# Performance work log

Hardware: AMD Instinct MI355X
Metric: run time of the kernel (lower is better)

Reference implementation:

```python
import jax, jax.numpy as jnp
import numpy as np

DPITCH_RANGE = 24.0
SCALE = 1.0


def setup_inputs() -> dict:
    key = jax.random.key(0)
    ks = jax.random.split(key, 10)
    B, T, ND, SD, H = 512, 1024, 64, 3, 256
    inp_size = ND + SD  # 67
    w = lambda k, shape: (jax.random.normal(k, shape, jnp.float32) * 0.05)
    return {
        "noise": jax.random.normal(ks[0], (B, T, ND), jnp.float32),
        "gap_duration": jax.random.uniform(ks[1], (B, T + 1, SD - 1), dtype=jnp.float32),
        "W_ih": w(ks[2], (4 * H, inp_size)),
        "W_hh": w(ks[3], (4 * H, H)),
        "b_ih": w(ks[4], (4 * H,)),
        "b_hh": w(ks[5], (4 * H,)),
        "W1": w(ks[6], (H, H)),
        "b1": w(ks[7], (H,)),
        "W2": w(ks[8], (1, H)),
        "b2": w(ks[9], (1,)),
    }


def reference(noise, gap_duration, W_ih, W_hh, b_ih, b_hh, W1, b1, W2, b2):
    B, T, _ = noise.shape
    H = W_hh.shape[1]

    def head(out):  # Linear -> Tanh -> Linear -> Tanh, scaled to deltapitch
        hdn = jnp.tanh(out @ W1.T + b1)
        return jnp.tanh(hdn @ W2.T + b2) * (DPITCH_RANGE * SCALE)

    def lstm_cell(h, c, x):  # torch LSTM gate order: i, f, g, o
        gates = x @ W_ih.T + b_ih + h @ W_hh.T + b_hh
        i, f, g, o = jnp.split(gates, 4, axis=-1)
        c = jax.nn.sigmoid(f) * c + jax.nn.sigmoid(i) * jnp.tanh(g)
        h = jax.nn.sigmoid(o) * jnp.tanh(c)
        return h, c

    def step(carry, inp):
        out, h, c = carry
        n_t, gap_t = inp  # [B, ND], [B, SD-1]
        x = jnp.concatenate([gap_t, head(out)], axis=-1)  # [B, SD]
        h, c = lstm_cell(h, c, jnp.concatenate([x, n_t], axis=-1))
        return (h, h, c), x

    z = jnp.zeros((B, H), noise.dtype)
    (out, _, _), xs = jax.lax.scan(
        step, (z, z, z),
        (noise.transpose(1, 0, 2), gap_duration[:, :T].transpose(1, 0, 2)))
    x_last = jnp.concatenate([gap_duration[:, T], head(out)], axis=-1)
    return jnp.concatenate([xs.transpose(1, 0, 2), x_last[:, None, :]], axis=1)
```

## Files before the change

### kernel.cpp

```cpp
#include <hip/hip_runtime.h>
#include <stdint.h>
#include <stddef.h>

typedef __bf16 bf16x8 __attribute__((ext_vector_type(8)));
typedef float f32x4 __attribute__((ext_vector_type(4)));

#define MFMA16(a, b, c) __builtin_amdgcn_mfma_f32_16x16x32_bf16((a), (b), (c), 0, 0, 0)

#define TSTEPS 1024
#define NDIM   64
#define NKC    10
#define NGT    64
#define MB     16
#define GROUPS 32
#define SLICES 8

#define GOFF    ((size_t)0)
#define GBYTES  ((size_t)NGT * NKC * 1024)
#define W1OFF   (GOFF + GBYTES)
#define W1BYTES ((size_t)16 * 8 * 1024)
#define BOFF    (W1OFF + W1BYTES)
#define XOFF    (BOFF + 4096)
#define XBYTES  ((size_t)256 * 2 * 512 * 4)
#define WSNEED  (XOFF + XBYTES)

__device__ __forceinline__ uint16_t f2bf(float f) {
    union { float f; uint32_t u; } v; v.f = f;
    return (uint16_t)((v.u + 0x7FFFu + ((v.u >> 16) & 1u)) >> 16);
}
__device__ __forceinline__ float fsig(float x) { return 1.0f / (1.0f + __expf(-x)); }
__device__ __forceinline__ float ftanh(float x) { return 2.0f / (1.0f + __expf(-2.0f * x)) - 1.0f; }

__device__ __forceinline__ void bar_lgkm() {
    asm volatile("s_waitcnt lgkmcnt(0)" ::: "memory");
    __builtin_amdgcn_s_barrier();
    asm volatile("" ::: "memory");
}

__global__ void prep_gates(const float* __restrict__ W_ih, const float* __restrict__ W_hh,
                           char* __restrict__ ws) {
    int F = blockIdx.x;
    int T = F / NKC, kc = F - T * NKC;
    int l = threadIdx.x;
    int row  = 16 * T + (l & 15);
    int unit = row >> 2, gt = row & 3;
    int orig = gt * 256 + unit;
    uint32_t w[4];
#pragma unroll
    for (int p = 0; p < 4; ++p) {
        float v[2];
#pragma unroll
        for (int e = 0; e < 2; ++e) {
            int k = 32 * kc + 8 * (l >> 4) + 2 * p + e;
            v[e] = (k < 64) ? W_ih[orig * 67 + 3 + k] : W_hh[orig * 256 + (k - 64)];
        }
        w[p] = (uint32_t)f2bf(v[0]) | ((uint32_t)f2bf(v[1]) << 16);
    }
    *(uint4*)(ws + GOFF + (size_t)F * 1024 + (size_t)l * 16) = make_uint4(w[0], w[1], w[2], w[3]);
}

__global__ void prep_w1(const float* __restrict__ W1, char* __restrict__ ws) {
    int F = blockIdx.x;
    int T = F / 8, kc = F - T * 8;
    int l = threadIdx.x;
    int row = 16 * T + (l & 15);
    uint32_t w[4];
#pragma unroll
    for (int p = 0; p < 4; ++p) {
        int k = 32 * kc + 8 * (l >> 4) + 2 * p;
        w[p] = (uint32_t)f2bf(W1[row * 256 + k]) | ((uint32_t)f2bf(W1[row * 256 + k + 1]) << 16);
    }
    *(uint4*)(ws + W1OFF + (size_t)F * 1024 + (size_t)l * 16) = make_uint4(w[0], w[1], w[2], w[3]);
}

__global__ void prep_small(const float* __restrict__ b_ih, const float* __restrict__ b_hh,
                           char* __restrict__ ws) {
    int t = threadIdx.x;
    float* sb = (float*)(ws + BOFF);
    if (t < 1024) {
        int unit = t >> 2, gt = t & 3;
        int orig = gt * 256 + unit;
        sb[t] = b_ih[orig] + b_hh[orig];
    }
}

__global__ __launch_bounds__(512, 2) void lstm_main(
        const float* __restrict__ noise, const float* __restrict__ gap,
        const float* __restrict__ W_ih, const float* __restrict__ b1p,
        const float* __restrict__ W2p, const float* __restrict__ b2p,
        char* __restrict__ ws, float* __restrict__ out) {
    __shared__ uint16_t act[MB * 320];
    __shared__ float dp_part[16][9];
    __shared__ float gxy[16][2];

    const int tid  = threadIdx.x;
    const int w    = tid >> 6;
    const int lane = tid & 63;
    const int q    = lane >> 4;
    const int col  = lane & 15;
    const int g    = blockIdx.x >> 3;
    const int s    = blockIdx.x & 7;
    const int b0   = g * MB;
    const int swz  = (col & 7) << 3;

    const uint4* gfr  = (const uint4*)(ws + GOFF);
    const uint4* w1fr = (const uint4*)(ws + W1OFF);
    const float* bias = (const float*)(ws + BOFF);
    uint32_t* pay = (uint32_t*)(ws + XOFF);

    for (int i = tid; i < MB * 320; i += 512) act[i] = 0;

    const int T = 8 * s + w;
    uint4 gw[NKC];
#pragma unroll
    for (int kc = 0; kc < NKC; ++kc) gw[kc] = gfr[(size_t)(T * NKC + kc) * 64 + lane];
    uint4 w1w[16];
#pragma unroll
    for (int i = 0; i < 2; ++i)
#pragma unroll
        for (int kc = 0; kc < 8; ++kc)
            w1w[i * 8 + kc] = w1fr[(size_t)((2 * w + i) * 8 + kc) * 64 + lane];

    const int rb = 16 * T + 4 * q;
    const float bI = bias[rb], bF = bias[rb + 1], bG = bias[rb + 2], bO = bias[rb + 3];
    float wx0[4], wx1[4], wx2[4];
#pragma unroll
    for (int r = 0; r < 4; ++r) {
        int row = rb + r;
        int orig = (row & 3) * 256 + (row >> 2);
        wx0[r] = W_ih[orig * 67 + 0];
        wx1[r] = W_ih[orig * 67 + 1];
        wx2[r] = W_ih[orig * 67 + 2] * 24.0f;
    }
    float b1r[8], w2r[8];
#pragma unroll
    for (int a = 0; a < 2; ++a)
#pragma unroll
        for (int r = 0; r < 4; ++r) {
            int row = 32 * w + 16 * a + 4 * q + r;
            b1r[4 * a + r] = b1p[row];
            w2r[4 * a + r] = W2p[row];
        }
    const float b2v = b2p[0];

    const int nbr = tid >> 5, nj = (tid & 31) * 2;
    const float* nptr = noise + (size_t)(b0 + nbr) * TSTEPS * NDIM + nj;
    float2 npf = *(const float2*)nptr;
    const bool xlead = (w == 7 && lane < 16);
    float2 gpf = make_float2(0.f, 0.f);
    if (xlead) gpf = *(const float2*)(gap + (size_t)(b0 + col) * (TSTEPS + 1) * 2);

    float creg = 0.f;
    const f32x4 fz = {0.f, 0.f, 0.f, 0.f};
    const int myidx = g * 8 + s;
    const int myunit = 32 * s + 4 * w + q;

    __syncthreads();

#pragma unroll 1
    for (int t = 0; t <= TSTEPS; ++t) {
        if (t < TSTEPS) {
            uint32_t nv = (uint32_t)f2bf(npf.x) | ((uint32_t)f2bf(npf.y) << 16);
            int sw = (nbr & 7) << 3;
            *(uint32_t*)&act[nbr * 320 + (nj ^ sw)] = nv;
            if (t + 1 < TSTEPS) npf = *(const float2*)(nptr + (size_t)(t + 1) * NDIM);
        }
        if (xlead) {
            gxy[col][0] = gpf.x; gxy[col][1] = gpf.y;
            if (s == 0) {
                float* o = out + ((size_t)(b0 + col) * (TSTEPS + 1) + t) * 3;
                o[0] = gpf.x; o[1] = gpf.y;
            }
            if (t < TSTEPS)
                gpf = *(const float2*)(gap + ((size_t)(b0 + col) * (TSTEPS + 1) + (t + 1)) * 2);
        }
        if (t > 0) {
            const unsigned tag = (unsigned)t;
            const int par = t & 1;
            unsigned pend = 0x7f;
            uint32_t vv[7];
            do {
#pragma unroll
                for (int pi = 0; pi < 7; ++pi)
                    if (pend & (1u << pi)) {
                        int p = (s + 1 + pi) & 7;
                        vv[pi] = __hip_atomic_load(
                            &pay[(((g * 8 + p) * 2 + par) << 9) + 64 * w + lane],
                            __ATOMIC_RELAXED, __HIP_MEMORY_SCOPE_AGENT);
                    }
#pragma unroll
                for (int pi = 0; pi < 7; ++pi)
                    if ((pend & (1u << pi)) && (vv[pi] >> 16) == tag) {
                        int p = (s + 1 + pi) & 7;
                        int u = 32 * p + 4 * w + q;
                        act[col * 320 + ((64 + u) ^ swz)] = (uint16_t)vv[pi];
                        pend &= ~(1u << pi);
                    }
            } while (pend);
        }
        bar_lgkm();

        f32x4 h0 = fz, h1 = fz;
#pragma unroll
        for (int kc = 0; kc < 8; ++kc) {
            bf16x8 bv = *(const bf16x8*)&act[col * 320 + ((64 + 32 * kc + 8 * q) ^ swz)];
            h0 = MFMA16(__builtin_bit_cast(bf16x8, w1w[kc]),     bv, h0);
            h1 = MFMA16(__builtin_bit_cast(bf16x8, w1w[8 + kc]), bv, h1);
        }
        float part = 0.f;
#pragma unroll
        for (int r = 0; r < 4; ++r) {
            part += ftanh(h0[r] + b1r[r])     * w2r[r];
            part += ftanh(h1[r] + b1r[4 + r]) * w2r[4 + r];
        }
        part += __shfl_xor(part, 16);
        part += __shfl_xor(part, 32);
        if (q == 0) dp_part[col][w] = part;
        bar_lgkm();

        const float* dpp = &dp_part[col][0];
        float inner = b2v + ((dpp[0] + dpp[1]) + (dpp[2] + dpp[3]))
                          + ((dpp[4] + dpp[5]) + (dpp[6] + dpp[7]));
        float tdp = ftanh(inner);

        if (t == TSTEPS) {
            if (s == 0 && w == 0 && q == 0)
                out[((size_t)(b0 + col) * (TSTEPS + 1) + t) * 3 + 2] = 24.0f * tdp;
            break;
        }

        f32x4 ga = fz;
#pragma unroll
        for (int kc = 0; kc < NKC; ++kc) {
            bf16x8 bv = *(const bf16x8*)&act[col * 320 + ((32 * kc + 8 * q) ^ swz)];
            ga = MFMA16(__builtin_bit_cast(bf16x8, gw[kc]), bv, ga);
        }
        const float g0 = gxy[col][0], g1 = gxy[col][1];
        float ii = ga[0] + bI + wx0[0] * g0 + wx1[0] * g1 + wx2[0] * tdp;
        float ff = ga[1] + bF + wx0[1] * g0 + wx1[1] * g1 + wx2[1] * tdp;
        float gg = ga[2] + bG + wx0[2] * g0 + wx1[2] * g1 + wx2[2] * tdp;
        float oo = ga[3] + bO + wx0[3] * g0 + wx1[3] * g1 + wx2[3] * tdp;
        float cn = fsig(ff) * creg + fsig(ii) * ftanh(gg);
        creg = cn;
        float hv = fsig(oo) * ftanh(cn);
        uint16_t hb = f2bf(hv);
        __hip_atomic_store(&pay[((myidx * 2 + ((t + 1) & 1)) << 9) + 64 * w + lane],
                           ((uint32_t)(t + 1) << 16) | (uint32_t)hb,
                           __ATOMIC_RELAXED, __HIP_MEMORY_SCOPE_AGENT);
        act[col * 320 + ((64 + myunit) ^ swz)] = hb;
        if (s == 0 && w == 0 && q == 0)
            out[((size_t)(b0 + col) * (TSTEPS + 1) + t) * 3 + 2] = 24.0f * tdp;
        bar_lgkm();
    }
}

extern "C" void kernel_launch(void* const* d_in, const int* in_sizes, int n_in,
                              void* d_out, int out_size, void* d_ws, size_t ws_size,
                              hipStream_t stream) {
    (void)in_sizes; (void)n_in; (void)out_size;
    if (ws_size < WSNEED) return;

    const float* noise = (const float*)d_in[0];
    const float* gap   = (const float*)d_in[1];
    const float* W_ih  = (const float*)d_in[2];
    const float* W_hh  = (const float*)d_in[3];
    const float* b_ih  = (const float*)d_in[4];
    const float* b_hh  = (const float*)d_in[5];
    const float* W1    = (const float*)d_in[6];
    const float* b1    = (const float*)d_in[7];
    const float* W2    = (const float*)d_in[8];
    const float* b2    = (const float*)d_in[9];
    char*  ws  = (char*)d_ws;
    float* out = (float*)d_out;

    hipMemsetAsync(ws + XOFF, 0, XBYTES, stream);
    hipLaunchKernelGGL(prep_gates, dim3(NGT * NKC), dim3(64), 0, stream, W_ih, W_hh, ws);
    hipLaunchKernelGGL(prep_w1,    dim3(16 * 8),    dim3(64), 0, stream, W1, ws);
    hipLaunchKernelGGL(prep_small, dim3(1), dim3(1024), 0, stream, b_ih, b_hh, ws);
    hipLaunchKernelGGL(lstm_main,  dim3(GROUPS * SLICES), dim3(512), 0, stream,
                       noise, gap, W_ih, b1, W2, b2, ws, out);
}
```

Before: 3.132 ms.

## Halve slices per batch group and double-buffer state to drop a barrier per step

Each batch group of 16 rows is now split across 4 workgroups instead of 8. Each wave computes two gate tiles, which cuts the number of peers each workgroup must poll per timestep from 7 to 3, and peer payloads are read as 64-bit atomic loads. The shared activation, noise, gap and partial buffers are double-buffered by timestep parity, so the barrier at the end of each step is removed and the head and gate MFMAs run in one interleaved loop. In exchange each workgroup does twice the gate MFMA work per step and holds more registers, and only 128 workgroups are launched.

After: 6.981 ms. 2.23x slower.

```diff
diff --git a/kernel.cpp b/kernel.cpp
--- a/kernel.cpp
+++ b/kernel.cpp
@@ -13,7 +13,7 @@
 #define NGT    64
 #define MB     16
 #define GROUPS 32
-#define SLICES 8
+#define SLICES 4
 
 #define GOFF    ((size_t)0)
 #define GBYTES  ((size_t)NGT * NKC * 1024)
@@ -21,8 +21,8 @@
 #define W1BYTES ((size_t)16 * 8 * 1024)
 #define BOFF    (W1OFF + W1BYTES)
 #define XOFF    (BOFF + 4096)
-#define XBYTES  ((size_t)256 * 2 * 512 * 4)
-#define WSNEED  (XOFF + XBYTES)
+#define PAYB    ((size_t)GROUPS * SLICES * 2 * 1024 * 4)
+#define WSNEED  (XOFF + PAYB)
 
 __device__ __forceinline__ uint16_t f2bf(float f) {
     union { float f; uint32_t u; } v; v.f = f;
@@ -89,17 +89,19 @@
         const float* __restrict__ W_ih, const float* __restrict__ b1p,
         const float* __restrict__ W2p, const float* __restrict__ b2p,
         char* __restrict__ ws, float* __restrict__ out) {
-    __shared__ uint16_t act[MB * 320];
-    __shared__ float dp_part[16][9];
-    __shared__ float gxy[16][2];
+    __shared__ uint16_t hfrag[2][16 * 256];
+    __shared__ uint16_t actn[2][16 * 64];
+    __shared__ float dp_part[2][16][9];
+    __shared__ float gxy[2][16][2];
 
     const int tid  = threadIdx.x;
     const int w    = tid >> 6;
     const int lane = tid & 63;
     const int q    = lane >> 4;
     const int col  = lane & 15;
-    const int g    = blockIdx.x >> 3;
-    const int s    = blockIdx.x & 7;
+    const int n    = blockIdx.x;
+    const int g    = n >> 2;
+    const int s    = n & 3;
     const int b0   = g * MB;
     const int swz  = (col & 7) << 3;
 
@@ -108,12 +110,15 @@
     const float* bias = (const float*)(ws + BOFF);
     uint32_t* pay = (uint32_t*)(ws + XOFF);
 
-    for (int i = tid; i < MB * 320; i += 512) act[i] = 0;
-
-    const int T = 8 * s + w;
-    uint4 gw[NKC];
-#pragma unroll
-    for (int kc = 0; kc < NKC; ++kc) gw[kc] = gfr[(size_t)(T * NKC + kc) * 64 + lane];
+    for (int i = tid; i < 16 * 256; i += 512) hfrag[0][i] = 0;
+
+    const int T0 = 16 * s + 2 * w;
+    uint4 gw0[NKC], gw1[NKC];
+#pragma unroll
+    for (int kc = 0; kc < NKC; ++kc) {
+        gw0[kc] = gfr[(size_t)(T0 * NKC + kc) * 64 + lane];
+        gw1[kc] = gfr[(size_t)((T0 + 1) * NKC + kc) * 64 + lane];
+    }
     uint4 w1w[16];
 #pragma unroll
     for (int i = 0; i < 2; ++i)
@@ -121,16 +126,19 @@
         for (int kc = 0; kc < 8; ++kc)
             w1w[i * 8 + kc] = w1fr[(size_t)((2 * w + i) * 8 + kc) * 64 + lane];
 
-    const int rb = 16 * T + 4 * q;
-    const float bI = bias[rb], bF = bias[rb + 1], bG = bias[rb + 2], bO = bias[rb + 3];
-    float wx0[4], wx1[4], wx2[4];
-#pragma unroll
-    for (int r = 0; r < 4; ++r) {
-        int row = rb + r;
-        int orig = (row & 3) * 256 + (row >> 2);
-        wx0[r] = W_ih[orig * 67 + 0];
-        wx1[r] = W_ih[orig * 67 + 1];
-        wx2[r] = W_ih[orig * 67 + 2] * 24.0f;
+    float bb[2][4], wxa[2][4], wxb[2][4], wxc[2][4];
+#pragma unroll
+    for (int i = 0; i < 2; ++i) {
+        int rb = 256 * s + 16 * (2 * w + i) + 4 * q;
+#pragma unroll
+        for (int r = 0; r < 4; ++r) {
+            int row = rb + r;
+            int orig = (row & 3) * 256 + (row >> 2);
+            bb[i][r]  = bias[row];
+            wxa[i][r] = W_ih[orig * 67 + 0];
+            wxb[i][r] = W_ih[orig * 67 + 1];
+            wxc[i][r] = W_ih[orig * 67 + 2] * 24.0f;
+        }
     }
     float b1r[8], w2r[8];
 #pragma unroll
@@ -143,69 +151,91 @@
         }
     const float b2v = b2p[0];
 
+    int pbase[3], ps[3];
+#pragma unroll
+    for (int p = 0; p < 3; ++p) {
+        ps[p] = (s + 1 + p) & 3;
+        pbase[p] = ((g * 4 + ps[p]) * 2) << 10;
+    }
+    const int mybase = ((g * 4 + s) * 2) << 10;
+    const int lu0 = 8 * w + q, lu1 = 8 * w + 4 + q;
+
     const int nbr = tid >> 5, nj = (tid & 31) * 2;
+    const int nsw = (nbr & 7) << 3;
     const float* nptr = noise + (size_t)(b0 + nbr) * TSTEPS * NDIM + nj;
     float2 npf = *(const float2*)nptr;
     const bool xlead = (w == 7 && lane < 16);
     float2 gpf = make_float2(0.f, 0.f);
     if (xlead) gpf = *(const float2*)(gap + (size_t)(b0 + col) * (TSTEPS + 1) * 2);
 
-    float creg = 0.f;
+    float creg[2] = {0.f, 0.f};
     const f32x4 fz = {0.f, 0.f, 0.f, 0.f};
-    const int myidx = g * 8 + s;
-    const int myunit = 32 * s + 4 * w + q;
 
     __syncthreads();
 
 #pragma unroll 1
     for (int t = 0; t <= TSTEPS; ++t) {
+        const int par = t & 1;
+        const uint32_t tg = (uint32_t)t;
+        const int parw = par << 10;
+
         if (t < TSTEPS) {
             uint32_t nv = (uint32_t)f2bf(npf.x) | ((uint32_t)f2bf(npf.y) << 16);
-            int sw = (nbr & 7) << 3;
-            *(uint32_t*)&act[nbr * 320 + (nj ^ sw)] = nv;
-            if (t + 1 < TSTEPS) npf = *(const float2*)(nptr + (size_t)(t + 1) * NDIM);
+            *(uint32_t*)&actn[par][(nbr * 64 + nj) ^ nsw] = nv;
         }
         if (xlead) {
-            gxy[col][0] = gpf.x; gxy[col][1] = gpf.y;
+            gxy[par][col][0] = gpf.x; gxy[par][col][1] = gpf.y;
             if (s == 0) {
                 float* o = out + ((size_t)(b0 + col) * (TSTEPS + 1) + t) * 3;
                 o[0] = gpf.x; o[1] = gpf.y;
             }
-            if (t < TSTEPS)
-                gpf = *(const float2*)(gap + ((size_t)(b0 + col) * (TSTEPS + 1) + (t + 1)) * 2);
         }
         if (t > 0) {
-            const unsigned tag = (unsigned)t;
-            const int par = t & 1;
-            unsigned pend = 0x7f;
-            uint32_t vv[7];
+            unsigned long long pv[3];
+            unsigned pend = 0x7;
             do {
 #pragma unroll
-                for (int pi = 0; pi < 7; ++pi)
-                    if (pend & (1u << pi)) {
-                        int p = (s + 1 + pi) & 7;
-                        vv[pi] = __hip_atomic_load(
-                            &pay[(((g * 8 + p) * 2 + par) << 9) + 64 * w + lane],
+                for (int p = 0; p < 3; ++p)
+                    if (pend & (1u << p)) {
+                        unsigned long long v = __hip_atomic_load(
+                            (const unsigned long long*)&pay[pbase[p] + parw + 2 * tid],
                             __ATOMIC_RELAXED, __HIP_MEMORY_SCOPE_AGENT);
-                    }
-#pragma unroll
-                for (int pi = 0; pi < 7; ++pi)
-                    if ((pend & (1u << pi)) && (vv[pi] >> 16) == tag) {
-                        int p = (s + 1 + pi) & 7;
-                        int u = 32 * p + 4 * w + q;
-                        act[col * 320 + ((64 + u) ^ swz)] = (uint16_t)vv[pi];
-                        pend &= ~(1u << pi);
+                        if ((((uint32_t)(v >> 16)) & 0xffffu) == tg &&
+                            ((uint32_t)(v >> 48)) == tg) {
+                            pv[p] = v; pend &= ~(1u << p);
+                        }
                     }
             } while (pend);
-        }
+            const int ru = tid >> 3;
+            const int rc0 = 2 * (tid & 7);
+#pragma unroll
+            for (int p = 0; p < 3; ++p) {
+                int gu = 64 * ps[p] + ru;
+                hfrag[par][(rc0 * 256 + gu) ^ ((rc0 & 7) << 3)]           = (uint16_t)pv[p];
+                hfrag[par][((rc0 + 1) * 256 + gu) ^ (((rc0 + 1) & 7) << 3)] = (uint16_t)(pv[p] >> 32);
+            }
+        }
+        if (t + 1 < TSTEPS) npf = *(const float2*)(nptr + (size_t)(t + 1) * NDIM);
+        if (xlead && t < TSTEPS)
+            gpf = *(const float2*)(gap + ((size_t)(b0 + col) * (TSTEPS + 1) + (t + 1)) * 2);
         bar_lgkm();
 
-        f32x4 h0 = fz, h1 = fz;
-#pragma unroll
-        for (int kc = 0; kc < 8; ++kc) {
-            bf16x8 bv = *(const bf16x8*)&act[col * 320 + ((64 + 32 * kc + 8 * q) ^ swz)];
-            h0 = MFMA16(__builtin_bit_cast(bf16x8, w1w[kc]),     bv, h0);
-            h1 = MFMA16(__builtin_bit_cast(bf16x8, w1w[8 + kc]), bv, h1);
+        f32x4 ga0 = fz, ga1 = fz, h0 = fz, h1 = fz;
+        {
+            bf16x8 bn0 = *(const bf16x8*)&actn[par][(col * 64 + 8 * q) ^ swz];
+            bf16x8 bn1 = *(const bf16x8*)&actn[par][(col * 64 + 32 + 8 * q) ^ swz];
+            ga0 = MFMA16(__builtin_bit_cast(bf16x8, gw0[0]), bn0, ga0);
+            ga0 = MFMA16(__builtin_bit_cast(bf16x8, gw0[1]), bn1, ga0);
+            ga1 = MFMA16(__builtin_bit_cast(bf16x8, gw1[0]), bn0, ga1);
+            ga1 = MFMA16(__builtin_bit_cast(bf16x8, gw1[1]), bn1, ga1);
+        }
+#pragma unroll
+        for (int c = 0; c < 8; ++c) {
+            bf16x8 bv = *(const bf16x8*)&hfrag[par][(col * 256 + 32 * c + 8 * q) ^ swz];
+            ga0 = MFMA16(__builtin_bit_cast(bf16x8, gw0[2 + c]), bv, ga0);
+            ga1 = MFMA16(__builtin_bit_cast(bf16x8, gw1[2 + c]), bv, ga1);
+            h0  = MFMA16(__builtin_bit_cast(bf16x8, w1w[c]),     bv, h0);
+            h1  = MFMA16(__builtin_bit_cast(bf16x8, w1w[8 + c]), bv, h1);
         }
         float part = 0.f;
 #pragma unroll
@@ -215,42 +245,37 @@
         }
         part += __shfl_xor(part, 16);
         part += __shfl_xor(part, 32);
-        if (q == 0) dp_part[col][w] = part;
+        if (q == 0) dp_part[par][col][w] = part;
         bar_lgkm();
 
-        const float* dpp = &dp_part[col][0];
+        const float* dpp = &dp_part[par][col][0];
         float inner = b2v + ((dpp[0] + dpp[1]) + (dpp[2] + dpp[3]))
                           + ((dpp[4] + dpp[5]) + (dpp[6] + dpp[7]));
         float tdp = ftanh(inner);
-
-        if (t == TSTEPS) {
-            if (s == 0 && w == 0 && q == 0)
-                out[((size_t)(b0 + col) * (TSTEPS + 1) + t) * 3 + 2] = 24.0f * tdp;
-            break;
-        }
-
-        f32x4 ga = fz;
-#pragma unroll
-        for (int kc = 0; kc < NKC; ++kc) {
-            bf16x8 bv = *(const bf16x8*)&act[col * 320 + ((32 * kc + 8 * q) ^ swz)];
-            ga = MFMA16(__builtin_bit_cast(bf16x8, gw[kc]), bv, ga);
-        }
-        const float g0 = gxy[col][0], g1 = gxy[col][1];
-        float ii = ga[0] + bI + wx0[0] * g0 + wx1[0] * g1 + wx2[0] * tdp;
-        float ff = ga[1] + bF + wx0[1] * g0 + wx1[1] * g1 + wx2[1] * tdp;
-        float gg = ga[2] + bG + wx0[2] * g0 + wx1[2] * g1 + wx2[2] * tdp;
-        float oo = ga[3] + bO + wx0[3] * g0 + wx1[3] * g1 + wx2[3] * tdp;
-        float cn = fsig(ff) * creg + fsig(ii) * ftanh(gg);
-        creg = cn;
-        float hv = fsig(oo) * ftanh(cn);
-        uint16_t hb = f2bf(hv);
-        __hip_atomic_store(&pay[((myidx * 2 + ((t + 1) & 1)) << 9) + 64 * w + lane],
-                           ((uint32_t)(t + 1) << 16) | (uint32_t)hb,
-                           __ATOMIC_RELAXED, __HIP_MEMORY_SCOPE_AGENT);
-        act[col * 320 + ((64 + myunit) ^ swz)] = hb;
-        if (s == 0 && w == 0 && q == 0)
+        if (s == 0 && w == 0 && lane < 16)
             out[((size_t)(b0 + col) * (TSTEPS + 1) + t) * 3 + 2] = 24.0f * tdp;
-        bar_lgkm();
+        if (t == TSTEPS) break;
+
+        const float g0 = gxy[par][col][0], g1 = gxy[par][col][1];
+        const int npar = (t + 1) & 1;
+        const uint32_t ntag = (uint32_t)(t + 1) << 16;
+#pragma unroll
+        for (int i = 0; i < 2; ++i) {
+            const f32x4& ga = i ? ga1 : ga0;
+            float ii = ga[0] + bb[i][0] + wxa[i][0] * g0 + wxb[i][0] * g1 + wxc[i][0] * tdp;
+            float ff = ga[1] + bb[i][1] + wxa[i][1] * g0 + wxb[i][1] * g1 + wxc[i][1] * tdp;
+            float gg = ga[2] + bb[i][2] + wxa[i][2] * g0 + wxb[i][2] * g1 + wxc[i][2] * tdp;
+            float oo = ga[3] + bb[i][3] + wxa[i][3] * g0 + wxb[i][3] * g1 + wxc[i][3] * tdp;
+            float cn = fsig(ff) * creg[i] + fsig(ii) * ftanh(gg);
+            creg[i] = cn;
+            float hv = fsig(oo) * ftanh(cn);
+            uint16_t hb = f2bf(hv);
+            int lu = i ? lu1 : lu0;
+            __hip_atomic_store(&pay[mybase + (npar << 10) + lu * 16 + col],
+                               ntag | (uint32_t)hb,
+                               __ATOMIC_RELAXED, __HIP_MEMORY_SCOPE_AGENT);
+            hfrag[npar][(col * 256 + 64 * s + lu) ^ swz] = hb;
+        }
     }
 }
 
@@ -273,7 +298,7 @@
     char*  ws  = (char*)d_ws;
     float* out = (float*)d_out;
 
-    hipMemsetAsync(ws + XOFF, 0, XBYTES, stream);
+    hipMemsetAsync(ws + XOFF, 0, PAYB, stream);
     hipLaunchKernelGGL(prep_gates, dim3(NGT * NKC), dim3(64), 0, stream, W_ih, W_hh, ws);
     hipLaunchKernelGGL(prep_w1,    dim3(16 * 8),    dim3(64), 0, stream, W1, ws);
     hipLaunchKernelGGL(prep_small, dim3(1), dim3(1024), 0, stream, b_ih, b_hh, ws);
```

## Interleave gate MFMAs with head MFMAs and drop per-step trailing barrier

Applied to the files above, without the earlier changes.

The LSTM gate matrix-multiply chain is moved ahead of the head reduction and interleaved with the W1 MFMAs, so both dependency chains share the same LDS operand loads and overlap. The gap staging buffer is double-buffered by step parity, which allows the barrier at the end of each step to be removed. Output writes are deferred by one step and done together after the peer-exchange poll, and the global prefetches for noise and gap are moved after the poll. This shortens the serial per-step critical path of the recurrence, at the cost of more live registers and more careful LDS hazard reasoning.

New measurement: 3.136 ms. About the same (+0.2%).

```diff
diff --git a/kernel.cpp b/kernel.cpp
--- a/kernel.cpp
+++ b/kernel.cpp
@@ -91,7 +91,7 @@
         char* __restrict__ ws, float* __restrict__ out) {
     __shared__ uint16_t act[MB * 320];
     __shared__ float dp_part[16][9];
-    __shared__ float gxy[16][2];
+    __shared__ float gxy[2][16][2];
 
     const int tid  = threadIdx.x;
     const int w    = tid >> 6;
@@ -147,10 +147,12 @@
     const float* nptr = noise + (size_t)(b0 + nbr) * TSTEPS * NDIM + nj;
     float2 npf = *(const float2*)nptr;
     const bool xlead = (w == 7 && lane < 16);
+    const bool olead = (s == 0 && w == 0);
     float2 gpf = make_float2(0.f, 0.f);
     if (xlead) gpf = *(const float2*)(gap + (size_t)(b0 + col) * (TSTEPS + 1) * 2);
 
     float creg = 0.f;
+    float o_g0 = 0.f, o_g1 = 0.f, o_tdp = 0.f;
     const f32x4 fz = {0.f, 0.f, 0.f, 0.f};
     const int myidx = g * 8 + s;
     const int myunit = 32 * s + 4 * w + q;
@@ -159,24 +161,17 @@
 
 #pragma unroll 1
     for (int t = 0; t <= TSTEPS; ++t) {
+        const int par = t & 1;
+        const uint32_t tg = (uint32_t)t;
+
         if (t < TSTEPS) {
             uint32_t nv = (uint32_t)f2bf(npf.x) | ((uint32_t)f2bf(npf.y) << 16);
             int sw = (nbr & 7) << 3;
             *(uint32_t*)&act[nbr * 320 + (nj ^ sw)] = nv;
-            if (t + 1 < TSTEPS) npf = *(const float2*)(nptr + (size_t)(t + 1) * NDIM);
-        }
-        if (xlead) {
-            gxy[col][0] = gpf.x; gxy[col][1] = gpf.y;
-            if (s == 0) {
-                float* o = out + ((size_t)(b0 + col) * (TSTEPS + 1) + t) * 3;
-                o[0] = gpf.x; o[1] = gpf.y;
-            }
-            if (t < TSTEPS)
-                gpf = *(const float2*)(gap + ((size_t)(b0 + col) * (TSTEPS + 1) + (t + 1)) * 2);
-        }
+        }
+        if (xlead) { gxy[par][col][0] = gpf.x; gxy[par][col][1] = gpf.y; }
+
         if (t > 0) {
-            const unsigned tag = (unsigned)t;
-            const int par = t & 1;
             unsigned pend = 0x7f;
             uint32_t vv[7];
             do {
@@ -190,20 +185,34 @@
                     }
 #pragma unroll
                 for (int pi = 0; pi < 7; ++pi)
-                    if ((pend & (1u << pi)) && (vv[pi] >> 16) == tag) {
+                    if ((pend & (1u << pi)) && (vv[pi] >> 16) == tg) {
                         int p = (s + 1 + pi) & 7;
                         int u = 32 * p + 4 * w + q;
                         act[col * 320 + ((64 + u) ^ swz)] = (uint16_t)vv[pi];
                         pend &= ~(1u << pi);
                     }
             } while (pend);
-        }
+            if (olead && q == 0) {
+                float* o = out + ((size_t)(b0 + col) * (TSTEPS + 1) + (t - 1)) * 3;
+                o[0] = o_g0; o[1] = o_g1; o[2] = 24.0f * o_tdp;
+            }
+        }
+        if (t + 1 < TSTEPS) npf = *(const float2*)(nptr + (size_t)(t + 1) * NDIM);
+        if (xlead && t < TSTEPS)
+            gpf = *(const float2*)(gap + ((size_t)(b0 + col) * (TSTEPS + 1) + (t + 1)) * 2);
         bar_lgkm();
 
-        f32x4 h0 = fz, h1 = fz;
+        f32x4 h0 = fz, h1 = fz, ga = fz;
+        {
+            bf16x8 bn0 = *(const bf16x8*)&act[col * 320 + ((8 * q) ^ swz)];
+            bf16x8 bn1 = *(const bf16x8*)&act[col * 320 + ((32 + 8 * q) ^ swz)];
+            ga = MFMA16(__builtin_bit_cast(bf16x8, gw[0]), bn0, ga);
+            ga = MFMA16(__builtin_bit_cast(bf16x8, gw[1]), bn1, ga);
+        }
 #pragma unroll
         for (int kc = 0; kc < 8; ++kc) {
             bf16x8 bv = *(const bf16x8*)&act[col * 320 + ((64 + 32 * kc + 8 * q) ^ swz)];
+            ga = MFMA16(__builtin_bit_cast(bf16x8, gw[2 + kc]), bv, ga);
             h0 = MFMA16(__builtin_bit_cast(bf16x8, w1w[kc]),     bv, h0);
             h1 = MFMA16(__builtin_bit_cast(bf16x8, w1w[8 + kc]), bv, h1);
         }
@@ -222,20 +231,17 @@
         float inner = b2v + ((dpp[0] + dpp[1]) + (dpp[2] + dpp[3]))
                           + ((dpp[4] + dpp[5]) + (dpp[6] + dpp[7]));
         float tdp = ftanh(inner);
+        const float g0 = gxy[par][col][0], g1 = gxy[par][col][1];
+        o_g0 = g0; o_g1 = g1; o_tdp = tdp;
 
         if (t == TSTEPS) {
-            if (s == 0 && w == 0 && q == 0)
-                out[((size_t)(b0 + col) * (TSTEPS + 1) + t) * 3 + 2] = 24.0f * tdp;
+            if (olead && q == 0) {
+                float* o = out + ((size_t)(b0 + col) * (TSTEPS + 1) + t) * 3;
+                o[0] = g0; o[1] = g1; o[2] = 24.0f * tdp;
+            }
             break;
         }
 
-        f32x4 ga = fz;
-#pragma unroll
-        for (int kc = 0; kc < NKC; ++kc) {
-            bf16x8 bv = *(const bf16x8*)&act[col * 320 + ((32 * kc + 8 * q) ^ swz)];
-            ga = MFMA16(__builtin_bit_cast(bf16x8, gw[kc]), bv, ga);
-        }
-        const float g0 = gxy[col][0], g1 = gxy[col][1];
         float ii = ga[0] + bI + wx0[0] * g0 + wx1[0] * g1 + wx2[0] * tdp;
         float ff = ga[1] + bF + wx0[1] * g0 + wx1[1] * g1 + wx2[1] * tdp;
         float gg = ga[2] + bG + wx0[2] * g0 + wx1[2] * g1 + wx2[2] * tdp;
@@ -248,9 +254,6 @@
                            ((uint32_t)(t + 1) << 16) | (uint32_t)hb,
                            __ATOMIC_RELAXED, __HIP_MEMORY_SCOPE_AGENT);
         act[col * 320 + ((64 + myunit) ^ swz)] = hb;
-        if (s == 0 && w == 0 && q == 0)
-            out[((size_t)(b0 + col) * (TSTEPS + 1) + t) * 3 + 2] = 24.0f * tdp;
-        bar_lgkm();
     }
 }
 
```
